# Kernel optimization log

Measured on AMD Instinct MI355X. Metric: run time of the kernel, lower is better.

## Reference

```python
import jax, jax.numpy as jnp
import numpy as np

B, L, H = 32, 512, 1024
Q = 128
VA_H = 256

def setup_inputs() -> dict:
    key = jax.random.key(0)
    ks = jax.random.split(key, 12)
    hidden_states = jax.random.normal(ks[0], (B, L, H), dtype=jnp.float32)
    # Build valid inclusive spans: start in [2, L-16), length in [0, 8)
    asp_s = jax.random.randint(ks[1], (B, Q), 2, L - 16)
    asp_e = asp_s + jax.random.randint(ks[2], (B, Q), 0, 8)
    opi_s = jax.random.randint(ks[3], (B, Q), 2, L - 16)
    opi_e = opi_s + jax.random.randint(ks[4], (B, Q), 0, 8)
    null = jax.random.uniform(ks[5], (B, Q)) < 0.1
    asp_s = jnp.where(null, 0, asp_s)
    quad_spans = jnp.stack([asp_s, asp_e, opi_s, opi_e], axis=-1).astype(jnp.int64)
    quad_mask = (jax.random.uniform(ks[6], (B, Q)) > 0.3).astype(jnp.float32)
    # MLP params (torch Linear: y = x @ W.T + b), kaiming-ish scale
    def lin(k, out_d, in_d):
        return jax.random.normal(k, (out_d, in_d), dtype=jnp.float32) / np.sqrt(in_d)
    W1 = lin(ks[7], VA_H, 3 * H); b1 = jnp.zeros((VA_H,), jnp.float32)
    W2 = lin(ks[8], VA_H // 2, VA_H); b2 = jnp.zeros((VA_H // 2,), jnp.float32)
    W3 = lin(ks[9], 2, VA_H // 2); b3 = jnp.zeros((2,), jnp.float32)
    return {"hidden_states": hidden_states, "quad_spans": quad_spans,
            "quad_mask": quad_mask, "W1": W1, "b1": b1, "W2": W2, "b2": b2,
            "W3": W3, "b3": b3}

def _pool_spans(hidden_states, s, e):
    # hidden_states: [B,L,H]; s,e: [B,Q] inclusive indices
    pos = jnp.arange(hidden_states.shape[1])  # [L]
    valid = (s >= 2) & (e >= s)               # [B,Q]
    m = (pos[None, None, :] >= s[..., None]) & (pos[None, None, :] <= e[..., None])
    m = (m & valid[..., None]).astype(hidden_states.dtype)  # [B,Q,L]
    cnt = jnp.maximum(m.sum(-1, keepdims=True), 1.0)        # [B,Q,1]
    mean = jnp.einsum('bql,blh->bqh', m, hidden_states) / cnt
    sep = hidden_states[:, 1:2, :]                           # [B,1,H] fallback
    return jnp.where(valid[..., None], mean, sep)

def reference(hidden_states, quad_spans, quad_mask, W1, b1, W2, b2, W3, b3):
    h_asp = _pool_spans(hidden_states, quad_spans[..., 0], quad_spans[..., 1])
    h_opi = _pool_spans(hidden_states, quad_spans[..., 2], quad_spans[..., 3])
    h_pair = jnp.concatenate([h_asp, h_opi, h_asp * h_opi], axis=-1)  # [B,Q,3H]
    x = jax.nn.gelu(h_pair @ W1.T + b1, approximate=False)  # torch GELU = erf
    x = jax.nn.gelu(x @ W2.T + b2, approximate=False)
    va = jax.nn.sigmoid(x @ W3.T + b3) * 8.0 + 1.0          # [B,Q,2] in [1,9]
    # Invalid pairs stay zero, matching the torch loop's skipped entries
    return va * (quad_mask >= 0.5).astype(va.dtype)[..., None]
```

## Files before the change

### kernel.cpp

```cpp
#include <hip/hip_runtime.h>
#include <hip/hip_bf16.h>
#include <math.h>

typedef __bf16 bf16x8 __attribute__((ext_vector_type(8)));
typedef float f32x4 __attribute__((ext_vector_type(4)));

__device__ __forceinline__ unsigned short f2bf(float x) {
    union { float f; unsigned int u; } v; v.f = x;
    unsigned int r = v.u + 0x7fffu + ((v.u >> 16) & 1u);
    return (unsigned short)(r >> 16);
}
__device__ __forceinline__ float gelu_exact(float v) {
    return 0.5f * v * (1.0f + erff(v * 0.70710678118654752f));
}

__global__ __launch_bounds__(256) void prep_kernel(const float* __restrict__ hs,
                                                   const int* __restrict__ spans,
                                                   const float* __restrict__ W1,
                                                   const float* __restrict__ W2,
                                                   unsigned short* __restrict__ hp,
                                                   unsigned short* __restrict__ w1b,
                                                   unsigned short* __restrict__ w2b) {
    const int blk = blockIdx.x;
    const int tid = threadIdx.x;

    if (blk >= 4096) {
        if (blk < 4864) {
            const int i = (blk - 4096) * 256 + tid;
            float4 f = ((const float4*)W1)[i];
            ushort4 u;
            u.x = f2bf(f.x); u.y = f2bf(f.y); u.z = f2bf(f.z); u.w = f2bf(f.w);
            ((ushort4*)w1b)[i] = u;
        } else {
            const int i = (blk - 4864) * 256 + tid;
            float4 f = ((const float4*)W2)[i];
            ushort4 u;
            u.x = f2bf(f.x); u.y = f2bf(f.y); u.z = f2bf(f.z); u.w = f2bf(f.w);
            ((ushort4*)w2b)[i] = u;
        }
        return;
    }

    const int pair = blk;
    const int b = pair >> 7;

    const bool is64 = (spans[1] == 0);
    int s_a, e_a, s_o, e_o;
    if (is64) {
        s_a = spans[(pair * 4 + 0) * 2]; e_a = spans[(pair * 4 + 1) * 2];
        s_o = spans[(pair * 4 + 2) * 2]; e_o = spans[(pair * 4 + 3) * 2];
    } else {
        s_a = spans[pair * 4 + 0]; e_a = spans[pair * 4 + 1];
        s_o = spans[pair * 4 + 2]; e_o = spans[pair * 4 + 3];
    }

    const float4* base = (const float4*)hs + (size_t)b * 512 * 256;

    float4 A, O;
    if (s_a >= 2 && e_a >= s_a) {
        float sx = 0.f, sy = 0.f, sz = 0.f, sw = 0.f;
        for (int t = s_a; t <= e_a; ++t) {
            float4 v = base[t * 256 + tid];
            sx += v.x; sy += v.y; sz += v.z; sw += v.w;
        }
        float inv = 1.0f / (float)(e_a - s_a + 1);
        A.x = sx * inv; A.y = sy * inv; A.z = sz * inv; A.w = sw * inv;
    } else {
        A = base[256 + tid];
    }
    if (s_o >= 2 && e_o >= s_o) {
        float sx = 0.f, sy = 0.f, sz = 0.f, sw = 0.f;
        for (int t = s_o; t <= e_o; ++t) {
            float4 v = base[t * 256 + tid];
            sx += v.x; sy += v.y; sz += v.z; sw += v.w;
        }
        float inv = 1.0f / (float)(e_o - s_o + 1);
        O.x = sx * inv; O.y = sy * inv; O.z = sz * inv; O.w = sw * inv;
    } else {
        O = base[256 + tid];
    }

    unsigned short* row = hp + (size_t)pair * 3072;
    const int d = tid * 4;
    ushort4 pa, po, pp;
    pa.x = f2bf(A.x); pa.y = f2bf(A.y); pa.z = f2bf(A.z); pa.w = f2bf(A.w);
    po.x = f2bf(O.x); po.y = f2bf(O.y); po.z = f2bf(O.z); po.w = f2bf(O.w);
    pp.x = f2bf(A.x * O.x); pp.y = f2bf(A.y * O.y);
    pp.z = f2bf(A.z * O.z); pp.w = f2bf(A.w * O.w);
    *(ushort4*)(row + d) = pa;
    *(ushort4*)(row + 1024 + d) = po;
    *(ushort4*)(row + 2048 + d) = pp;
}

__global__ __launch_bounds__(256, 2) void gemm1_gelu(const unsigned short* __restrict__ A,
                                                     const unsigned short* __restrict__ Bw,
                                                     const float* __restrict__ b1,
                                                     unsigned short* __restrict__ x1) {
    __shared__ __align__(16) unsigned short As[2][32 * 128];
    __shared__ __align__(16) unsigned short Bs[2][64 * 128];

    const int tid = threadIdx.x;
    const int lane = tid & 63;
    const int wid = tid >> 6;
    const int quad = lane >> 4;
    const int l16 = lane & 15;
    const int m0 = blockIdx.x * 32;
    const int n0 = blockIdx.y * 64;

    const int arow = tid >> 4;
    const int ac = tid & 15;
    const unsigned short* Aptr[2];
#pragma unroll
    for (int p = 0; p < 2; ++p) {
        const int row = arow + p * 16;
        const int lch = ((ac & 7) ^ (row & 7)) | (ac & 8);
        Aptr[p] = A + (size_t)(m0 + row) * 3072 + lch * 8;
    }
    const unsigned short* Bptr[4];
#pragma unroll
    for (int p = 0; p < 4; ++p) {
        const int row = arow + p * 16;
        const int lch = ((ac & 7) ^ (row & 7)) | (ac & 8);
        Bptr[p] = Bw + (size_t)(n0 + row) * 3072 + lch * 8;
    }

    int aoff[2][4], boff[4];
#pragma unroll
    for (int h = 0; h < 4; ++h) {
        const int c = h * 4 + quad;
#pragma unroll
        for (int mh = 0; mh < 2; ++mh) {
            const int row = mh * 16 + l16;
            const int pc = ((c & 7) ^ (row & 7)) | (c & 8);
            aoff[mh][h] = row * 128 + pc * 8;
        }
        const int brow = wid * 16 + l16;
        const int pcb = ((c & 7) ^ (brow & 7)) | (c & 8);
        boff[h] = brow * 128 + pcb * 8;
    }

    f32x4 acc[2] = {};

#pragma unroll
    for (int p = 0; p < 2; ++p)
        __builtin_amdgcn_global_load_lds(
            (const __attribute__((address_space(1))) void*)Aptr[p],
            (__attribute__((address_space(3))) void*)(&As[0][(p * 256 + tid) * 8]), 16, 0, 0);
#pragma unroll
    for (int p = 0; p < 4; ++p)
        __builtin_amdgcn_global_load_lds(
            (const __attribute__((address_space(1))) void*)Bptr[p],
            (__attribute__((address_space(3))) void*)(&Bs[0][(p * 256 + tid) * 8]), 16, 0, 0);

    for (int it = 0; it < 24; ++it) {
        const int cur = it & 1;
        __syncthreads();
        if (it + 1 < 24) {
            const int nxt = cur ^ 1;
            const int kadv = (it + 1) * 128;
#pragma unroll
            for (int p = 0; p < 2; ++p)
                __builtin_amdgcn_global_load_lds(
                    (const __attribute__((address_space(1))) void*)(Aptr[p] + kadv),
                    (__attribute__((address_space(3))) void*)(&As[nxt][(p * 256 + tid) * 8]), 16, 0, 0);
#pragma unroll
            for (int p = 0; p < 4; ++p)
                __builtin_amdgcn_global_load_lds(
                    (const __attribute__((address_space(1))) void*)(Bptr[p] + kadv),
                    (__attribute__((address_space(3))) void*)(&Bs[nxt][(p * 256 + tid) * 8]), 16, 0, 0);
        }
#pragma unroll
        for (int h = 0; h < 4; ++h) {
            bf16x8 b = *(const bf16x8*)&Bs[cur][boff[h]];
#pragma unroll
            for (int mh = 0; mh < 2; ++mh) {
                bf16x8 a = *(const bf16x8*)&As[cur][aoff[mh][h]];
                acc[mh] = __builtin_amdgcn_mfma_f32_16x16x32_bf16(a, b, acc[mh], 0, 0, 0);
            }
        }
    }

    const int n = n0 + wid * 16 + l16;
    const float bn = b1[n];
#pragma unroll
    for (int mh = 0; mh < 2; ++mh) {
#pragma unroll
        for (int rr = 0; rr < 4; ++rr) {
            const int m = m0 + mh * 16 + quad * 4 + rr;
            x1[(size_t)m * 256 + n] = f2bf(gelu_exact(acc[mh][rr] + bn));
        }
    }
}

__global__ __launch_bounds__(256) void mlp2_head(const unsigned short* __restrict__ x1,
                                                 const unsigned short* __restrict__ w2b,
                                                 const float* __restrict__ b2,
                                                 const float* __restrict__ W3,
                                                 const float* __restrict__ b3,
                                                 const float* __restrict__ mask,
                                                 float* __restrict__ out) {
    __shared__ __align__(16) unsigned short Xs[32][72];
    __shared__ __align__(16) unsigned short Ws[128][72];
    __shared__ float X2[32][132];

    const int tid = threadIdx.x;
    const int lane = tid & 63;
    const int wid = tid >> 6;
    const int wM = (wid >> 1) * 16;
    const int wN = (wid & 1) * 64;
    const int quad = lane >> 4;
    const int l16 = lane & 15;
    const int m0 = blockIdx.x * 32;

    f32x4 acc[4] = {};

    for (int k0 = 0; k0 < 256; k0 += 64) {
        {
            const int r = tid >> 3, c = (tid & 7) * 8;
            *(uint4*)&Xs[r][c] = *(const uint4*)(x1 + (size_t)(m0 + r) * 256 + k0 + c);
        }
#pragma unroll
        for (int p = 0; p < 4; ++p) {
            const int v = tid + p * 256;
            const int r = v >> 3, c = (v & 7) * 8;
            *(uint4*)&Ws[r][c] = *(const uint4*)(w2b + (size_t)r * 256 + k0 + c);
        }
        __syncthreads();
#pragma unroll
        for (int kk = 0; kk < 64; kk += 32) {
            bf16x8 a = *(const bf16x8*)&Xs[wM + l16][kk + quad * 8];
#pragma unroll
            for (int ni = 0; ni < 4; ++ni) {
                bf16x8 b = *(const bf16x8*)&Ws[wN + ni * 16 + l16][kk + quad * 8];
                acc[ni] = __builtin_amdgcn_mfma_f32_16x16x32_bf16(a, b, acc[ni], 0, 0, 0);
            }
        }
        __syncthreads();
    }

#pragma unroll
    for (int ni = 0; ni < 4; ++ni) {
        const int n = wN + ni * 16 + l16;
        const float bn = b2[n];
#pragma unroll
        for (int rr = 0; rr < 4; ++rr) {
            const int m = wM + quad * 4 + rr;
            X2[m][n] = gelu_exact(acc[ni][rr] + bn);
        }
    }
    __syncthreads();

    const int p = tid >> 3;
    const int cc = (tid & 7) * 16;
    float a0 = 0.f, a1 = 0.f;
#pragma unroll
    for (int j = 0; j < 16; ++j) {
        const float xv = X2[p][cc + j];
        a0 += xv * W3[cc + j];
        a1 += xv * W3[128 + cc + j];
    }
    a0 += __shfl_xor(a0, 1); a0 += __shfl_xor(a0, 2); a0 += __shfl_xor(a0, 4);
    a1 += __shfl_xor(a1, 1); a1 += __shfl_xor(a1, 2); a1 += __shfl_xor(a1, 4);
    if ((tid & 7) == 0) {
        const int pair = m0 + p;
        const float mk = (mask[pair] >= 0.5f) ? 1.0f : 0.0f;
        out[pair * 2 + 0] = ((1.0f / (1.0f + expf(-(a0 + b3[0])))) * 8.0f + 1.0f) * mk;
        out[pair * 2 + 1] = ((1.0f / (1.0f + expf(-(a1 + b3[1])))) * 8.0f + 1.0f) * mk;
    }
}

extern "C" void kernel_launch(void* const* d_in, const int* in_sizes, int n_in,
                              void* d_out, int out_size, void* d_ws, size_t ws_size,
                              hipStream_t stream) {
    const float* hs   = (const float*)d_in[0];
    const int*   spans= (const int*)d_in[1];
    const float* mask = (const float*)d_in[2];
    const float* W1   = (const float*)d_in[3];
    const float* b1   = (const float*)d_in[4];
    const float* W2   = (const float*)d_in[5];
    const float* b2   = (const float*)d_in[6];
    const float* W3   = (const float*)d_in[7];
    const float* b3   = (const float*)d_in[8];
    float* out = (float*)d_out;

    unsigned short* hp  = (unsigned short*)d_ws;
    unsigned short* w1b = (unsigned short*)((char*)d_ws + 25165824);
    unsigned short* x1  = (unsigned short*)((char*)d_ws + 26738688);
    unsigned short* w2b = (unsigned short*)((char*)d_ws + 28835840);

    prep_kernel<<<dim3(4896), dim3(256), 0, stream>>>(hs, spans, W1, W2, hp, w1b, w2b);
    gemm1_gelu<<<dim3(128, 4), dim3(256), 0, stream>>>(hp, w1b, b1, x1);
    mlp2_head<<<dim3(128), dim3(256), 0, stream>>>(x1, w2b, b2, W3, b3, mask, out);
}
```

Before: 148.7 us.

## Fuse second MLP layer and head into GEMM1 via last-block atomic counter

```diff
diff --git a/kernel.cpp b/kernel.cpp
--- a/kernel.cpp
+++ b/kernel.cpp
@@ -20,7 +20,8 @@
                                                    const float* __restrict__ W2,
                                                    unsigned short* __restrict__ hp,
                                                    unsigned short* __restrict__ w1b,
-                                                   unsigned short* __restrict__ w2b) {
+                                                   unsigned short* __restrict__ w2b,
+                                                   int* __restrict__ cnt) {
     const int blk = blockIdx.x;
     const int tid = threadIdx.x;
 
@@ -32,6 +33,7 @@
             u.x = f2bf(f.x); u.y = f2bf(f.y); u.z = f2bf(f.z); u.w = f2bf(f.w);
             ((ushort4*)w1b)[i] = u;
         } else {
+            if (blk == 4864 && tid < 128) cnt[tid] = 0;
             const int i = (blk - 4864) * 256 + tid;
             float4 f = ((const float4*)W2)[i];
             ushort4 u;
@@ -92,12 +94,21 @@
     *(ushort4*)(row + 2048 + d) = pp;
 }
 
-__global__ __launch_bounds__(256, 2) void gemm1_gelu(const unsigned short* __restrict__ A,
-                                                     const unsigned short* __restrict__ Bw,
-                                                     const float* __restrict__ b1,
-                                                     unsigned short* __restrict__ x1) {
-    __shared__ __align__(16) unsigned short As[2][32 * 128];
-    __shared__ __align__(16) unsigned short Bs[2][64 * 128];
+__global__ __launch_bounds__(256, 2) void gemm1_fused(const unsigned short* __restrict__ A,
+                                                      const unsigned short* __restrict__ Bw,
+                                                      const float* __restrict__ b1,
+                                                      unsigned short* __restrict__ x1,
+                                                      const unsigned short* __restrict__ w2b,
+                                                      const float* __restrict__ b2,
+                                                      const float* __restrict__ W3,
+                                                      const float* __restrict__ b3,
+                                                      const float* __restrict__ mask,
+                                                      float* __restrict__ out,
+                                                      int* __restrict__ cnt) {
+    __shared__ __align__(16) unsigned char smem[49152];
+    __shared__ int s_last;
+    unsigned short* As = (unsigned short*)smem;
+    unsigned short* Bs = (unsigned short*)(smem + 16384);
 
     const int tid = threadIdx.x;
     const int lane = tid & 63;
@@ -145,12 +156,12 @@
     for (int p = 0; p < 2; ++p)
         __builtin_amdgcn_global_load_lds(
             (const __attribute__((address_space(1))) void*)Aptr[p],
-            (__attribute__((address_space(3))) void*)(&As[0][(p * 256 + tid) * 8]), 16, 0, 0);
+            (__attribute__((address_space(3))) void*)(&As[(p * 256 + tid) * 8]), 16, 0, 0);
 #pragma unroll
     for (int p = 0; p < 4; ++p)
         __builtin_amdgcn_global_load_lds(
             (const __attribute__((address_space(1))) void*)Bptr[p],
-            (__attribute__((address_space(3))) void*)(&Bs[0][(p * 256 + tid) * 8]), 16, 0, 0);
+            (__attribute__((address_space(3))) void*)(&Bs[(p * 256 + tid) * 8]), 16, 0, 0);
 
     for (int it = 0; it < 24; ++it) {
         const int cur = it & 1;
@@ -162,90 +173,107 @@
             for (int p = 0; p < 2; ++p)
                 __builtin_amdgcn_global_load_lds(
                     (const __attribute__((address_space(1))) void*)(Aptr[p] + kadv),
-                    (__attribute__((address_space(3))) void*)(&As[nxt][(p * 256 + tid) * 8]), 16, 0, 0);
+                    (__attribute__((address_space(3))) void*)(&As[nxt * 4096 + (p * 256 + tid) * 8]), 16, 0, 0);
 #pragma unroll
             for (int p = 0; p < 4; ++p)
                 __builtin_amdgcn_global_load_lds(
                     (const __attribute__((address_space(1))) void*)(Bptr[p] + kadv),
-                    (__attribute__((address_space(3))) void*)(&Bs[nxt][(p * 256 + tid) * 8]), 16, 0, 0);
+                    (__attribute__((address_space(3))) void*)(&Bs[nxt * 8192 + (p * 256 + tid) * 8]), 16, 0, 0);
         }
 #pragma unroll
         for (int h = 0; h < 4; ++h) {
-            bf16x8 b = *(const bf16x8*)&Bs[cur][boff[h]];
+            bf16x8 b = *(const bf16x8*)&Bs[cur * 8192 + boff[h]];
 #pragma unroll
             for (int mh = 0; mh < 2; ++mh) {
-                bf16x8 a = *(const bf16x8*)&As[cur][aoff[mh][h]];
+                bf16x8 a = *(const bf16x8*)&As[cur * 4096 + aoff[mh][h]];
                 acc[mh] = __builtin_amdgcn_mfma_f32_16x16x32_bf16(a, b, acc[mh], 0, 0, 0);
             }
         }
     }
 
-    const int n = n0 + wid * 16 + l16;
-    const float bn = b1[n];
-#pragma unroll
-    for (int mh = 0; mh < 2; ++mh) {
+    {
+        const int n = n0 + wid * 16 + l16;
+        const float bn = b1[n];
+#pragma unroll
+        for (int mh = 0; mh < 2; ++mh) {
+#pragma unroll
+            for (int rr = 0; rr < 4; ++rr) {
+                const int m = m0 + mh * 16 + quad * 4 + rr;
+                unsigned short v = f2bf(gelu_exact(acc[mh][rr] + bn));
+                __hip_atomic_store(&x1[(size_t)m * 256 + n], v,
+                                   __ATOMIC_RELAXED, __HIP_MEMORY_SCOPE_AGENT);
+            }
+        }
+    }
+
+    __syncthreads();
+    if (tid == 0) {
+        __threadfence();
+        int old = __hip_atomic_fetch_add(&cnt[blockIdx.x], 1,
+                                         __ATOMIC_ACQ_REL, __HIP_MEMORY_SCOPE_AGENT);
+        s_last = (old == 3) ? 1 : 0;
+    }
+    __syncthreads();
+    if (!s_last) return;
+
+    unsigned short* Xs = (unsigned short*)smem;
+    unsigned short* Ws = (unsigned short*)(smem + 16384);
+    float* X2 = (float*)(smem + 32768);
+
+#pragma unroll
+    for (int p = 0; p < 16; ++p) {
+        const int s = p * 256 + tid;
+        const int row = s >> 7;
+        const int c = (s >> 2) & 31;
+        const int dw = s & 3;
+        unsigned int v = __hip_atomic_load(
+            (const unsigned int*)(x1 + (size_t)(m0 + row) * 256 + c * 8 + dw * 2),
+            __ATOMIC_RELAXED, __HIP_MEMORY_SCOPE_AGENT);
+        const int pc = ((c & 7) ^ (row & 7)) | (c & 24);
+        *(unsigned int*)&Xs[row * 256 + pc * 8 + dw * 2] = v;
+    }
+
+    const int wM2 = (wid >> 1) * 16;
+    const int wN2 = (wid & 1) * 64;
+    f32x4 acc2[4] = {};
+
+    for (int k0 = 0; k0 < 256; k0 += 64) {
+#pragma unroll
+        for (int p = 0; p < 4; ++p) {
+            const int s = p * 256 + tid;
+            const int row = s >> 3;
+            const int c = s & 7;
+            const int pc = c ^ (row & 7);
+            *(uint4*)&Ws[row * 64 + pc * 8] =
+                *(const uint4*)(w2b + (size_t)row * 256 + k0 + c * 8);
+        }
+        __syncthreads();
+#pragma unroll
+        for (int kk = 0; kk < 64; kk += 32) {
+            const int ca = (k0 + kk) / 8 + quad;
+            const int rowa = wM2 + l16;
+            const int pca = ((ca & 7) ^ (rowa & 7)) | (ca & 24);
+            bf16x8 a = *(const bf16x8*)&Xs[rowa * 256 + pca * 8];
+            const int cb = kk / 8 + quad;
+#pragma unroll
+            for (int ni = 0; ni < 4; ++ni) {
+                const int rowb = wN2 + ni * 16 + l16;
+                const int pcb = cb ^ (rowb & 7);
+                bf16x8 b = *(const bf16x8*)&Ws[rowb * 64 + pcb * 8];
+                acc2[ni] = __builtin_amdgcn_mfma_f32_16x16x32_bf16(a, b, acc2[ni], 0, 0, 0);
+            }
+        }
+        __syncthreads();
+    }
+
+#pragma unroll
+    for (int ni = 0; ni < 4; ++ni) {
+        const int n = wN2 + ni * 16 + l16;
+        const float bn = b2[n];
 #pragma unroll
         for (int rr = 0; rr < 4; ++rr) {
-            const int m = m0 + mh * 16 + quad * 4 + rr;
-            x1[(size_t)m * 256 + n] = f2bf(gelu_exact(acc[mh][rr] + bn));
-        }
-    }
-}
-
-__global__ __launch_bounds__(256) void mlp2_head(const unsigned short* __restrict__ x1,
-                                                 const unsigned short* __restrict__ w2b,
-                                                 const float* __restrict__ b2,
-                                                 const float* __restrict__ W3,
-                                                 const float* __restrict__ b3,
-                                                 const float* __restrict__ mask,
-                                                 float* __restrict__ out) {
-    __shared__ __align__(16) unsigned short Xs[32][72];
-    __shared__ __align__(16) unsigned short Ws[128][72];
-    __shared__ float X2[32][132];
-
-    const int tid = threadIdx.x;
-    const int lane = tid & 63;
-    const int wid = tid >> 6;
-    const int wM = (wid >> 1) * 16;
-    const int wN = (wid & 1) * 64;
-    const int quad = lane >> 4;
-    const int l16 = lane & 15;
-    const int m0 = blockIdx.x * 32;
-
-    f32x4 acc[4] = {};
-
-    for (int k0 = 0; k0 < 256; k0 += 64) {
-        {
-            const int r = tid >> 3, c = (tid & 7) * 8;
-            *(uint4*)&Xs[r][c] = *(const uint4*)(x1 + (size_t)(m0 + r) * 256 + k0 + c);
-        }
-#pragma unroll
-        for (int p = 0; p < 4; ++p) {
-            const int v = tid + p * 256;
-            const int r = v >> 3, c = (v & 7) * 8;
-            *(uint4*)&Ws[r][c] = *(const uint4*)(w2b + (size_t)r * 256 + k0 + c);
-        }
-        __syncthreads();
-#pragma unroll
-        for (int kk = 0; kk < 64; kk += 32) {
-            bf16x8 a = *(const bf16x8*)&Xs[wM + l16][kk + quad * 8];
-#pragma unroll
-            for (int ni = 0; ni < 4; ++ni) {
-                bf16x8 b = *(const bf16x8*)&Ws[wN + ni * 16 + l16][kk + quad * 8];
-                acc[ni] = __builtin_amdgcn_mfma_f32_16x16x32_bf16(a, b, acc[ni], 0, 0, 0);
-            }
-        }
-        __syncthreads();
-    }
-
-#pragma unroll
-    for (int ni = 0; ni < 4; ++ni) {
-        const int n = wN + ni * 16 + l16;
-        const float bn = b2[n];
-#pragma unroll
-        for (int rr = 0; rr < 4; ++rr) {
-            const int m = wM + quad * 4 + rr;
-            X2[m][n] = gelu_exact(acc[ni][rr] + bn);
+            const int m = wM2 + quad * 4 + rr;
+            X2[m * 128 + n] = gelu_exact(acc2[ni][rr] + bn);
         }
     }
     __syncthreads();
@@ -255,7 +283,7 @@
     float a0 = 0.f, a1 = 0.f;
 #pragma unroll
     for (int j = 0; j < 16; ++j) {
-        const float xv = X2[p][cc + j];
+        const float xv = X2[p * 128 + cc + j];
         a0 += xv * W3[cc + j];
         a1 += xv * W3[128 + cc + j];
     }
@@ -287,8 +315,9 @@
     unsigned short* w1b = (unsigned short*)((char*)d_ws + 25165824);
     unsigned short* x1  = (unsigned short*)((char*)d_ws + 26738688);
     unsigned short* w2b = (unsigned short*)((char*)d_ws + 28835840);
-
-    prep_kernel<<<dim3(4896), dim3(256), 0, stream>>>(hs, spans, W1, W2, hp, w1b, w2b);
-    gemm1_gelu<<<dim3(128, 4), dim3(256), 0, stream>>>(hp, w1b, b1, x1);
-    mlp2_head<<<dim3(128), dim3(256), 0, stream>>>(x1, w2b, b2, W3, b3, mask, out);
-}
+    int*            cnt = (int*)((char*)d_ws + 28901376);
+
+    prep_kernel<<<dim3(4896), dim3(256), 0, stream>>>(hs, spans, W1, W2, hp, w1b, w2b, cnt);
+    gemm1_fused<<<dim3(128, 4), dim3(256), 0, stream>>>(hp, w1b, b1, x1, w2b, b2,
+                                                        W3, b3, mask, out, cnt);
+}
```

After: 169.2 us. 13.8% more time.

## Widen GEMM1 K-tile to 192 and load full K in mlp2 via direct-to-LDS

Applied to the files above, without the earlier changes.

```diff
diff --git a/kernel.cpp b/kernel.cpp
--- a/kernel.cpp
+++ b/kernel.cpp
@@ -96,8 +96,8 @@
                                                      const unsigned short* __restrict__ Bw,
                                                      const float* __restrict__ b1,
                                                      unsigned short* __restrict__ x1) {
-    __shared__ __align__(16) unsigned short As[2][32 * 128];
-    __shared__ __align__(16) unsigned short Bs[2][64 * 128];
+    __shared__ __align__(16) unsigned short As[2 * 32 * 192];
+    __shared__ __align__(16) unsigned short Bs[2 * 64 * 192];
 
     const int tid = threadIdx.x;
     const int lane = tid & 63;
@@ -107,74 +107,76 @@
     const int m0 = blockIdx.x * 32;
     const int n0 = blockIdx.y * 64;
 
-    const int arow = tid >> 4;
-    const int ac = tid & 15;
-    const unsigned short* Aptr[2];
-#pragma unroll
-    for (int p = 0; p < 2; ++p) {
-        const int row = arow + p * 16;
-        const int lch = ((ac & 7) ^ (row & 7)) | (ac & 8);
+    const unsigned short* Aptr[3];
+#pragma unroll
+    for (int p = 0; p < 3; ++p) {
+        const int s = p * 256 + tid;
+        const int row = s / 24;
+        const int c = s - row * 24;
+        const int lch = (c & 24) | ((c & 7) ^ (row & 7));
         Aptr[p] = A + (size_t)(m0 + row) * 3072 + lch * 8;
     }
-    const unsigned short* Bptr[4];
-#pragma unroll
-    for (int p = 0; p < 4; ++p) {
-        const int row = arow + p * 16;
-        const int lch = ((ac & 7) ^ (row & 7)) | (ac & 8);
+    const unsigned short* Bptr[6];
+#pragma unroll
+    for (int p = 0; p < 6; ++p) {
+        const int s = p * 256 + tid;
+        const int row = s / 24;
+        const int c = s - row * 24;
+        const int lch = (c & 24) | ((c & 7) ^ (row & 7));
         Bptr[p] = Bw + (size_t)(n0 + row) * 3072 + lch * 8;
     }
 
-    int aoff[2][4], boff[4];
-#pragma unroll
-    for (int h = 0; h < 4; ++h) {
+    int aoff[2][6], boff[6];
+#pragma unroll
+    for (int h = 0; h < 6; ++h) {
         const int c = h * 4 + quad;
 #pragma unroll
         for (int mh = 0; mh < 2; ++mh) {
             const int row = mh * 16 + l16;
-            const int pc = ((c & 7) ^ (row & 7)) | (c & 8);
-            aoff[mh][h] = row * 128 + pc * 8;
+            const int pc = (c & 24) | ((c & 7) ^ (row & 7));
+            aoff[mh][h] = row * 192 + pc * 8;
         }
         const int brow = wid * 16 + l16;
-        const int pcb = ((c & 7) ^ (brow & 7)) | (c & 8);
-        boff[h] = brow * 128 + pcb * 8;
+        const int pcb = (c & 24) | ((c & 7) ^ (brow & 7));
+        boff[h] = brow * 192 + pcb * 8;
     }
 
     f32x4 acc[2] = {};
 
 #pragma unroll
-    for (int p = 0; p < 2; ++p)
+    for (int p = 0; p < 3; ++p)
         __builtin_amdgcn_global_load_lds(
             (const __attribute__((address_space(1))) void*)Aptr[p],
-            (__attribute__((address_space(3))) void*)(&As[0][(p * 256 + tid) * 8]), 16, 0, 0);
-#pragma unroll
-    for (int p = 0; p < 4; ++p)
+            (__attribute__((address_space(3))) void*)(&As[(p * 256 + tid) * 8]), 16, 0, 0);
+#pragma unroll
+    for (int p = 0; p < 6; ++p)
         __builtin_amdgcn_global_load_lds(
             (const __attribute__((address_space(1))) void*)Bptr[p],
-            (__attribute__((address_space(3))) void*)(&Bs[0][(p * 256 + tid) * 8]), 16, 0, 0);
-
-    for (int it = 0; it < 24; ++it) {
+            (__attribute__((address_space(3))) void*)(&Bs[(p * 256 + tid) * 8]), 16, 0, 0);
+
+    for (int it = 0; it < 16; ++it) {
         const int cur = it & 1;
         __syncthreads();
-        if (it + 1 < 24) {
+        if (it + 1 < 16) {
             const int nxt = cur ^ 1;
-            const int kadv = (it + 1) * 128;
-#pragma unroll
-            for (int p = 0; p < 2; ++p)
+            const int kadv = (it + 1) * 192;
+#pragma unroll
+            for (int p = 0; p < 3; ++p)
                 __builtin_amdgcn_global_load_lds(
                     (const __attribute__((address_space(1))) void*)(Aptr[p] + kadv),
-                    (__attribute__((address_space(3))) void*)(&As[nxt][(p * 256 + tid) * 8]), 16, 0, 0);
-#pragma unroll
-            for (int p = 0; p < 4; ++p)
+                    (__attribute__((address_space(3))) void*)(&As[nxt * 6144 + (p * 256 + tid) * 8]), 16, 0, 0);
+#pragma unroll
+            for (int p = 0; p < 6; ++p)
                 __builtin_amdgcn_global_load_lds(
                     (const __attribute__((address_space(1))) void*)(Bptr[p] + kadv),
-                    (__attribute__((address_space(3))) void*)(&Bs[nxt][(p * 256 + tid) * 8]), 16, 0, 0);
-        }
-#pragma unroll
-        for (int h = 0; h < 4; ++h) {
-            bf16x8 b = *(const bf16x8*)&Bs[cur][boff[h]];
+                    (__attribute__((address_space(3))) void*)(&Bs[nxt * 12288 + (p * 256 + tid) * 8]), 16, 0, 0);
+        }
+#pragma unroll
+        for (int h = 0; h < 6; ++h) {
+            bf16x8 b = *(const bf16x8*)&Bs[cur * 12288 + boff[h]];
 #pragma unroll
             for (int mh = 0; mh < 2; ++mh) {
-                bf16x8 a = *(const bf16x8*)&As[cur][aoff[mh][h]];
+                bf16x8 a = *(const bf16x8*)&As[cur * 6144 + aoff[mh][h]];
                 acc[mh] = __builtin_amdgcn_mfma_f32_16x16x32_bf16(a, b, acc[mh], 0, 0, 0);
             }
         }
@@ -199,43 +201,56 @@
                                                  const float* __restrict__ b3,
                                                  const float* __restrict__ mask,
                                                  float* __restrict__ out) {
-    __shared__ __align__(16) unsigned short Xs[32][72];
-    __shared__ __align__(16) unsigned short Ws[128][72];
-    __shared__ float X2[32][132];
+    __shared__ __align__(16) unsigned char smem[98304];
+    unsigned short* Xs = (unsigned short*)smem;
+    unsigned short* Ws = (unsigned short*)(smem + 16384);
+    float*          X2 = (float*)(smem + 81920);
 
     const int tid = threadIdx.x;
     const int lane = tid & 63;
     const int wid = tid >> 6;
+    const int quad = lane >> 4;
+    const int l16 = lane & 15;
     const int wM = (wid >> 1) * 16;
     const int wN = (wid & 1) * 64;
-    const int quad = lane >> 4;
-    const int l16 = lane & 15;
     const int m0 = blockIdx.x * 32;
 
+#pragma unroll
+    for (int p = 0; p < 4; ++p) {
+        const int s = p * 256 + tid;
+        const int row = s >> 5;
+        const int c = s & 31;
+        const int lch = (c & 24) | ((c & 7) ^ (row & 7));
+        __builtin_amdgcn_global_load_lds(
+            (const __attribute__((address_space(1))) void*)(x1 + (size_t)(m0 + row) * 256 + lch * 8),
+            (__attribute__((address_space(3))) void*)(&Xs[s * 8]), 16, 0, 0);
+    }
+#pragma unroll
+    for (int p = 0; p < 16; ++p) {
+        const int s = p * 256 + tid;
+        const int row = s >> 5;
+        const int c = s & 31;
+        const int lch = (c & 24) | ((c & 7) ^ (row & 7));
+        __builtin_amdgcn_global_load_lds(
+            (const __attribute__((address_space(1))) void*)(w2b + (size_t)row * 256 + lch * 8),
+            (__attribute__((address_space(3))) void*)(&Ws[s * 8]), 16, 0, 0);
+    }
+    __syncthreads();
+
     f32x4 acc[4] = {};
-
-    for (int k0 = 0; k0 < 256; k0 += 64) {
-        {
-            const int r = tid >> 3, c = (tid & 7) * 8;
-            *(uint4*)&Xs[r][c] = *(const uint4*)(x1 + (size_t)(m0 + r) * 256 + k0 + c);
-        }
-#pragma unroll
-        for (int p = 0; p < 4; ++p) {
-            const int v = tid + p * 256;
-            const int r = v >> 3, c = (v & 7) * 8;
-            *(uint4*)&Ws[r][c] = *(const uint4*)(w2b + (size_t)r * 256 + k0 + c);
-        }
-        __syncthreads();
-#pragma unroll
-        for (int kk = 0; kk < 64; kk += 32) {
-            bf16x8 a = *(const bf16x8*)&Xs[wM + l16][kk + quad * 8];
-#pragma unroll
-            for (int ni = 0; ni < 4; ++ni) {
-                bf16x8 b = *(const bf16x8*)&Ws[wN + ni * 16 + l16][kk + quad * 8];
-                acc[ni] = __builtin_amdgcn_mfma_f32_16x16x32_bf16(a, b, acc[ni], 0, 0, 0);
-            }
-        }
-        __syncthreads();
+#pragma unroll
+    for (int h = 0; h < 8; ++h) {
+        const int c = h * 4 + quad;
+        const int rowa = wM + l16;
+        const int pca = (c & 24) | ((c & 7) ^ (rowa & 7));
+        bf16x8 a = *(const bf16x8*)&Xs[rowa * 256 + pca * 8];
+#pragma unroll
+        for (int ni = 0; ni < 4; ++ni) {
+            const int rowb = wN + ni * 16 + l16;
+            const int pcb = (c & 24) | ((c & 7) ^ (rowb & 7));
+            bf16x8 b = *(const bf16x8*)&Ws[rowb * 256 + pcb * 8];
+            acc[ni] = __builtin_amdgcn_mfma_f32_16x16x32_bf16(a, b, acc[ni], 0, 0, 0);
+        }
     }
 
 #pragma unroll
@@ -245,7 +260,7 @@
 #pragma unroll
         for (int rr = 0; rr < 4; ++rr) {
             const int m = wM + quad * 4 + rr;
-            X2[m][n] = gelu_exact(acc[ni][rr] + bn);
+            X2[m * 128 + n] = gelu_exact(acc[ni][rr] + bn);
         }
     }
     __syncthreads();
@@ -255,7 +270,7 @@
     float a0 = 0.f, a1 = 0.f;
 #pragma unroll
     for (int j = 0; j < 16; ++j) {
-        const float xv = X2[p][cc + j];
+        const float xv = X2[p * 128 + cc + j];
         a0 += xv * W3[cc + j];
         a1 += xv * W3[128 + cc + j];
     }
```

Result: no change. 146.3 us, median of 2 (-1.6%).
